# Kernel tuning notes

Measured on AMD Instinct MI355X. Metric: run time of the kernel, lower is better.

Reference implementation:

```python
import jax, jax.numpy as jnp
import numpy as np

N_NODES = 100000
N_EDGES = 1000000
F = 64
ALPHA = 0.1
BETA = 0.5


def setup_inputs() -> dict:
    key = jax.random.key(0)
    k1, k2, k3, k4, k5, k6 = jax.random.split(key, 6)
    features = jax.random.normal(k1, (N_NODES, F), dtype=jnp.float32)
    features0 = jax.random.normal(k2, (N_NODES, F), dtype=jnp.float32)
    edge_src = jax.random.randint(k3, (N_EDGES,), 0, N_NODES, dtype=jnp.int32)
    edge_dst = jax.random.randint(k4, (N_EDGES,), 0, N_NODES, dtype=jnp.int32)
    edge_vals = jax.random.uniform(k5, (N_EDGES,), dtype=jnp.float32)
    W = jax.random.normal(k6, (F, F), dtype=jnp.float32) * (1.0 / np.sqrt(F))
    return {"features": features, "features0": features0, "edge_src": edge_src,
            "edge_dst": edge_dst, "edge_vals": edge_vals, "W": W}


def reference(features, features0, edge_src, edge_dst, edge_vals, W):
    # hi = A @ features  (sparse propagation via edge-list segment sum)
    msgs = features[edge_src] * edge_vals[:, None]           # [E, F]
    hi = jax.ops.segment_sum(msgs, edge_dst, num_segments=N_NODES)  # [N, F]
    # variant=False branch of GCNII-style layer
    support = (1.0 - ALPHA) * hi + ALPHA * features0          # [N, F]
    r = support
    output = BETA * (support @ W) + (1.0 - BETA) * r          # [N, F]
    return jax.nn.relu(output)
```

## Files before the change

### kernel.cpp

```cpp
#include <hip/hip_runtime.h>

#define N_NODES 100000
#define N_EDGES 1000000
#define FDIM    64
#define TILES   6250
#define CAP     36
#define LBS     37

#define MM_BLOCKS  512
#define EPB        4096
#define BIN_BLOCKS ((N_EDGES + EPB - 1) / EPB)

#define NPART  512
#define PNODES 196
#define PCAP   2560

#define SCAN_BLOCKS 391

#define B_GCUR  0u
#define B_BKT   4096u
#define B_PRE   10489856u
#define B_GBF   23289856u
#define B_NEED  36100000u

#define C_DEG    0u
#define C_OFFS   409600u
#define C_CURSOR 819200u
#define C_BSUM   1228800u
#define C_BOFF   1232896u
#define C_BPACK  1236992u
#define C_PRE    5242880u
#define C_GBF    18042880u

typedef short bf16x8 __attribute__((ext_vector_type(8)));
typedef float f32x4  __attribute__((ext_vector_type(4)));

__device__ __forceinline__ short f2bf(float f) {
    unsigned u = __float_as_uint(f);
    u += 0x7fff + ((u >> 16) & 1);
    return (short)(u >> 16);
}

__device__ __forceinline__ unsigned packrec(int s, float v) {
    unsigned q = (unsigned)__float2int_rn(v * 32768.0f);
    q = q > 32767u ? 32767u : q;
    return ((unsigned)s << 15) | q;
}

__device__ __forceinline__ int part_of(int d) {
    return (int)(((unsigned)(d >> 2) * 171197u) >> 23);
}

__global__ __launch_bounds__(512, 4) void k_fused(
        const float* __restrict__ feat, const float* __restrict__ f0,
        const float* __restrict__ W, unsigned short* __restrict__ gbf,
        unsigned short* __restrict__ preBf,
        const int* __restrict__ src, const int* __restrict__ dst,
        const float* __restrict__ val,
        unsigned* __restrict__ bkt, int* __restrict__ gcur, int binBlocks) {

    if ((int)blockIdx.x < binBlocks) {
        __shared__ int            hist[512];
        __shared__ int            excl[512];
        __shared__ int            curs[512];
        __shared__ int            gbas[512];
        __shared__ int            wsum[8];
        __shared__ unsigned short slotpid[EPB];
        __shared__ uint2          rbuf[EPB];

        int t = threadIdx.x;
        hist[t] = 0;
        __syncthreads();

        int e0 = blockIdx.x * EPB + t * 8;
        unsigned recx[8]; int dd[8]; int pid[8];
        bool vld = e0 < N_EDGES;
        if (vld) {
            int4   sa = *(const int4*)(src + e0);
            int4   sb = *(const int4*)(src + e0 + 4);
            int4   da = *(const int4*)(dst + e0);
            int4   db = *(const int4*)(dst + e0 + 4);
            float4 va = *(const float4*)(val + e0);
            float4 vb = *(const float4*)(val + e0 + 4);
            int   s8[8] = {sa.x, sa.y, sa.z, sa.w, sb.x, sb.y, sb.z, sb.w};
            int   d8[8] = {da.x, da.y, da.z, da.w, db.x, db.y, db.z, db.w};
            float v8[8] = {va.x, va.y, va.z, va.w, vb.x, vb.y, vb.z, vb.w};
#pragma unroll
            for (int j = 0; j < 8; ++j) {
                recx[j] = packrec(s8[j], v8[j]);
                dd[j]   = d8[j];
                pid[j]  = part_of(d8[j]);
            }
#pragma unroll
            for (int j = 0; j < 8; ++j)
                atomicAdd(&hist[pid[j]], 1);
        }
        __syncthreads();

        int myv  = hist[t];
        int lanev = myv;
#pragma unroll
        for (int off = 1; off < 64; off <<= 1) {
            int nv = __shfl_up(lanev, off, 64);
            if ((t & 63) >= off) lanev += nv;
        }
        if ((t & 63) == 63) wsum[t >> 6] = lanev;
        __syncthreads();
        int prev = 0, total = 0;
#pragma unroll
        for (int w = 0; w < 8; ++w) {
            int s = wsum[w];
            prev  += (w < (t >> 6)) ? s : 0;
            total += s;
        }
        int ex = lanev + prev - myv;
        excl[t] = ex;
        curs[t] = ex;
        gbas[t] = (myv > 0) ? atomicAdd(&gcur[t], myv) : 0;
        __syncthreads();

        if (vld) {
#pragma unroll
            for (int j = 0; j < 8; ++j) {
                int pos = atomicAdd(&curs[pid[j]], 1);
                rbuf[pos]    = make_uint2(recx[j], (unsigned)dd[j]);
                slotpid[pos] = (unsigned short)pid[j];
            }
        }
        __syncthreads();

        uint2* pbuf = (uint2*)bkt;
        for (int i = t; i < total; i += 512) {
            int p   = slotpid[i];
            int off = gbas[p] + (i - excl[p]);
            if (off < PCAP)
                pbuf[(size_t)p * PCAP + off] = rbuf[i];
        }
        return;
    }

    int lane = threadIdx.x & 63;
    int mmb  = blockIdx.x - binBlocks;
    int wid  = mmb * 8 + (threadIdx.x >> 6);
    int nw   = (gridDim.x - binBlocks) * 8;
    int n16  = lane & 15, q = lane >> 4;

    bf16x8 bf[2][4];
#pragma unroll
    for (int s = 0; s < 2; ++s)
#pragma unroll
        for (int t = 0; t < 4; ++t) {
            bf16x8 b;
#pragma unroll
            for (int j = 0; j < 8; ++j) {
                int k = 32 * s + 8 * q + j, n = 16 * t + n16;
                float m = 0.5f * W[k * FDIM + n] + (k == n ? 0.5f : 0.0f);
                b[j] = f2bf(m);
            }
            bf[s][t] = b;
        }

    for (int tid = wid; tid < 2 * TILES; tid += nw) {
        bool hpath = tid >= TILES;
        int  row0  = (hpath ? tid - TILES : tid) * 16;
        const float* x = (hpath ? f0 : feat) + (size_t)row0 * FDIM;

        bf16x8 af[2];
#pragma unroll
        for (int s = 0; s < 2; ++s) {
            const float* xp = x + (size_t)n16 * FDIM + 32 * s + 8 * q;
            float4 u0 = *(const float4*)xp;
            float4 u1 = *(const float4*)(xp + 4);
            bf16x8 a;
            a[0] = f2bf(u0.x); a[1] = f2bf(u0.y); a[2] = f2bf(u0.z); a[3] = f2bf(u0.w);
            a[4] = f2bf(u1.x); a[5] = f2bf(u1.y); a[6] = f2bf(u1.z); a[7] = f2bf(u1.w);
            af[s] = a;
        }

        f32x4 acc[4] = {{0,0,0,0},{0,0,0,0},{0,0,0,0},{0,0,0,0}};
#pragma unroll
        for (int s = 0; s < 2; ++s)
#pragma unroll
            for (int t = 0; t < 4; ++t)
                acc[t] = __builtin_amdgcn_mfma_f32_16x16x32_bf16(af[s], bf[s][t], acc[t], 0, 0, 0);

        if (!hpath) {
#pragma unroll
            for (int t = 0; t < 4; ++t)
#pragma unroll
                for (int r = 0; r < 4; ++r)
                    gbf[(size_t)(row0 + 4 * q + r) * FDIM + 16 * t + n16] =
                        (unsigned short)f2bf(acc[t][r]);
        } else {
#pragma unroll
            for (int t = 0; t < 4; ++t)
#pragma unroll
                for (int r = 0; r < 4; ++r)
                    preBf[(size_t)(row0 + 4 * q + r) * FDIM + 16 * t + n16] =
                        (unsigned short)f2bf(0.1f * acc[t][r]);
        }
    }
}

__global__ __launch_bounds__(1024, 8) void k_pg(
        const unsigned* __restrict__ bkt, const int* __restrict__ gcur,
        const unsigned short* __restrict__ gbf,
        const unsigned short* __restrict__ preBf, float* __restrict__ out) {
    __shared__ int      lcnt[PNODES];
    __shared__ unsigned lbkt[PNODES * LBS];

    int p = blockIdx.x, t = threadIdx.x;
    int p196 = p * PNODES;

    for (int i = t; i < PNODES; i += 1024) lcnt[i] = 0;
    __syncthreads();

    int nE = gcur[p];
    if (nE > PCAP) nE = PCAP;
    const uint2* pb = (const uint2*)bkt + (size_t)p * PCAP;
    for (int e = t; e < nE; e += 1024) {
        uint2 r  = pb[e];
        int   ld = (int)r.y - p196;
        int  pos = atomicAdd(&lcnt[ld], 1);
        if (pos < CAP) lbkt[ld * LBS + pos] = r.x;
    }
    __syncthreads();

    int lane = t & 63, w = t >> 6;
    int fl = lane & 15, sub = lane >> 4;

    for (int ld0 = 2 * w; ld0 < PNODES; ld0 += 32) {
        int ld1   = ld0 + 1;
        int node0 = p196 + ld0;
        int node1 = p196 + ld1;
        if (node0 >= N_NODES) break;
        bool has1 = node1 < N_NODES;

        int c0 = lcnt[ld0];
        int deg0 = __builtin_amdgcn_readfirstlane(c0 < CAP ? c0 : CAP);
        int c1 = has1 ? lcnt[ld1] : 0;
        int deg1 = __builtin_amdgcn_readfirstlane(c1 < CAP ? c1 : CAP);
        int mdeg = deg0 > deg1 ? deg0 : deg1;

        uint2 hp0 = ((const uint2*)(preBf + (size_t)node0 * FDIM))[fl];
        uint2 hp1 = ((const uint2*)(preBf +
                       (size_t)(has1 ? node1 : node0) * FDIM))[fl];

        float a0 = 0, a1 = 0, a2 = 0, a3 = 0;
        float b0 = 0, b1 = 0, b2 = 0, b3 = 0;

        for (int e0 = 0; e0 < mdeg; e0 += 16) {
            unsigned rr0[4], rr1[4];
#pragma unroll
            for (int j = 0; j < 4; ++j) {
                int idx = e0 + 4 * j + sub;
                rr0[j] = (idx < deg0) ? lbkt[ld0 * LBS + idx] : 0u;
                rr1[j] = (idx < deg1) ? lbkt[ld1 * LBS + idx] : 0u;
            }
            uint2 u0[4], u1[4];
#pragma unroll
            for (int j = 0; j < 4; ++j) {
                u0[j] = ((const uint2*)(gbf + (size_t)(rr0[j] >> 15) * FDIM))[fl];
                u1[j] = ((const uint2*)(gbf + (size_t)(rr1[j] >> 15) * FDIM))[fl];
            }
#pragma unroll
            for (int j = 0; j < 4; ++j) {
                float v0 = (float)(rr0[j] & 0x7fffu) * (1.0f / 32768.0f);
                float v1 = (float)(rr1[j] & 0x7fffu) * (1.0f / 32768.0f);
                a0 = fmaf(v0, __uint_as_float(u0[j].x << 16),         a0);
                a1 = fmaf(v0, __uint_as_float(u0[j].x & 0xffff0000u), a1);
                a2 = fmaf(v0, __uint_as_float(u0[j].y << 16),         a2);
                a3 = fmaf(v0, __uint_as_float(u0[j].y & 0xffff0000u), a3);
                b0 = fmaf(v1, __uint_as_float(u1[j].x << 16),         b0);
                b1 = fmaf(v1, __uint_as_float(u1[j].x & 0xffff0000u), b1);
                b2 = fmaf(v1, __uint_as_float(u1[j].y << 16),         b2);
                b3 = fmaf(v1, __uint_as_float(u1[j].y & 0xffff0000u), b3);
            }
        }
        a0 += __shfl_xor(a0, 16); a0 += __shfl_xor(a0, 32);
        a1 += __shfl_xor(a1, 16); a1 += __shfl_xor(a1, 32);
        a2 += __shfl_xor(a2, 16); a2 += __shfl_xor(a2, 32);
        a3 += __shfl_xor(a3, 16); a3 += __shfl_xor(a3, 32);
        b0 += __shfl_xor(b0, 16); b0 += __shfl_xor(b0, 32);
        b1 += __shfl_xor(b1, 16); b1 += __shfl_xor(b1, 32);
        b2 += __shfl_xor(b2, 16); b2 += __shfl_xor(b2, 32);
        b3 += __shfl_xor(b3, 16); b3 += __shfl_xor(b3, 32);
        if (sub == 0) {
            float4 r4;
            r4.x = fmaxf(0.9f * a0 + __uint_as_float(hp0.x << 16),         0.0f);
            r4.y = fmaxf(0.9f * a1 + __uint_as_float(hp0.x & 0xffff0000u), 0.0f);
            r4.z = fmaxf(0.9f * a2 + __uint_as_float(hp0.y << 16),         0.0f);
            r4.w = fmaxf(0.9f * a3 + __uint_as_float(hp0.y & 0xffff0000u), 0.0f);
            ((float4*)(out + (size_t)node0 * FDIM))[fl] = r4;
            if (has1) {
                float4 s4;
                s4.x = fmaxf(0.9f * b0 + __uint_as_float(hp1.x << 16),         0.0f);
                s4.y = fmaxf(0.9f * b1 + __uint_as_float(hp1.x & 0xffff0000u), 0.0f);
                s4.z = fmaxf(0.9f * b2 + __uint_as_float(hp1.y << 16),         0.0f);
                s4.w = fmaxf(0.9f * b3 + __uint_as_float(hp1.y & 0xffff0000u), 0.0f);
                ((float4*)(out + (size_t)node1 * FDIM))[fl] = s4;
            }
        }
    }
}

__device__ __forceinline__ void gather_core(int node, int lane,
                                            const unsigned* base, int deg,
                                            const unsigned short* gbf,
                                            const unsigned short* preBf,
                                            float* out) {
    int fl  = lane & 31;
    int sub = lane >> 5;

    unsigned hp = ((const unsigned*)(preBf + (size_t)node * FDIM))[fl];
    float accLo = 0.0f, accHi = 0.0f;

    for (int e0 = 0; e0 < deg; e0 += 16) {
        unsigned rsel[8];
        float    vsel[8];
#pragma unroll
        for (int j = 0; j < 8; ++j) {
            int i0 = e0 + 2 * j, i1 = i0 + 1;
            int c0 = i0 < deg ? i0 : deg - 1;
            int c1 = i1 < deg ? i1 : deg - 1;
            unsigned rA = base[c0];
            unsigned rB = base[c1];
            unsigned r  = sub ? rB : rA;
            bool ok = (sub ? i1 : i0) < deg;
            rsel[j] = r;
            vsel[j] = ok ? (float)(r & 0x7fffu) * (1.0f / 32768.0f) : 0.0f;
        }
        unsigned u[8];
#pragma unroll
        for (int j = 0; j < 8; ++j)
            u[j] = *(const unsigned*)(gbf + (size_t)(rsel[j] >> 15) * FDIM + 2 * fl);
#pragma unroll
        for (int j = 0; j < 8; ++j) {
            accLo = fmaf(vsel[j], __uint_as_float(u[j] << 16), accLo);
            accHi = fmaf(vsel[j], __uint_as_float(u[j] & 0xffff0000u), accHi);
        }
    }
    accLo += __shfl_xor(accLo, 32);
    accHi += __shfl_xor(accHi, 32);
    if (sub == 0) {
        float2 r2;
        r2.x = fmaxf(0.9f * accLo + __uint_as_float(hp << 16), 0.0f);
        r2.y = fmaxf(0.9f * accHi + __uint_as_float(hp & 0xffff0000u), 0.0f);
        ((float2*)(out + (size_t)node * FDIM))[fl] = r2;
    }
}

__global__ __launch_bounds__(256, 8) void k_gather_c(
        const int* __restrict__ offs, const unsigned* __restrict__ bpack,
        const unsigned short* __restrict__ gbf,
        const unsigned short* __restrict__ preBf, float* __restrict__ out) {
    int gid  = blockIdx.x * blockDim.x + threadIdx.x;
    int node = __builtin_amdgcn_readfirstlane(gid >> 6);
    int lane = threadIdx.x & 63;
    if (node >= N_NODES) return;
    int beg = __builtin_amdgcn_readfirstlane(offs[node]);
    int end = __builtin_amdgcn_readfirstlane(
        (node == N_NODES - 1) ? N_EDGES : offs[node + 1]);
    gather_core(node, lane, bpack + beg, end - beg, gbf, preBf, out);
}

__global__ void k_hist(const int* __restrict__ dst, int* __restrict__ deg) {
    int e = blockIdx.x * blockDim.x + threadIdx.x;
    if (e < N_EDGES) atomicAdd(&deg[dst[e]], 1);
}

__global__ void k_scan1(const int* __restrict__ deg, int* __restrict__ bsum) {
    __shared__ int lds[256];
    int i = blockIdx.x * 256 + threadIdx.x;
    lds[threadIdx.x] = (i < N_NODES) ? deg[i] : 0;
    __syncthreads();
    for (int s = 128; s > 0; s >>= 1) {
        if (threadIdx.x < s) lds[threadIdx.x] += lds[threadIdx.x + s];
        __syncthreads();
    }
    if (threadIdx.x == 0) bsum[blockIdx.x] = lds[0];
}

__global__ void k_scan2(const int* __restrict__ bsum, int* __restrict__ boff) {
    __shared__ int lds[512];
    int t = threadIdx.x;
    int v = (t < SCAN_BLOCKS) ? bsum[t] : 0;
    lds[t] = v;
    __syncthreads();
    for (int off = 1; off < 512; off <<= 1) {
        int add = (t >= off) ? lds[t - off] : 0;
        __syncthreads();
        lds[t] += add;
        __syncthreads();
    }
    if (t < SCAN_BLOCKS) boff[t] = lds[t] - v;
}

__global__ void k_scan3(const int* __restrict__ deg, const int* __restrict__ boff,
                        int* __restrict__ offs, int* __restrict__ cursor) {
    __shared__ int lds[256];
    int t = threadIdx.x;
    int i = blockIdx.x * 256 + t;
    int v = (i < N_NODES) ? deg[i] : 0;
    lds[t] = v;
    __syncthreads();
    for (int off = 1; off < 256; off <<= 1) {
        int add = (t >= off) ? lds[t - off] : 0;
        __syncthreads();
        lds[t] += add;
        __syncthreads();
    }
    int excl = lds[t] - v + boff[blockIdx.x];
    if (i < N_NODES) { offs[i] = excl; cursor[i] = excl; }
}

__global__ void k_bin_c(const int* __restrict__ src, const int* __restrict__ dst,
                        const float* __restrict__ val, int* __restrict__ cursor,
                        unsigned* __restrict__ bpack) {
    int e = blockIdx.x * blockDim.x + threadIdx.x;
    if (e >= N_EDGES) return;
    int d = dst[e];
    int p = atomicAdd(&cursor[d], 1);
    bpack[p] = packrec(src[e], val[e]);
}

extern "C" void kernel_launch(void* const* d_in, const int* in_sizes, int n_in,
                              void* d_out, int out_size, void* d_ws, size_t ws_size,
                              hipStream_t stream) {
    const float* features  = (const float*)d_in[0];
    const float* features0 = (const float*)d_in[1];
    const int*   edge_src  = (const int*)d_in[2];
    const int*   edge_dst  = (const int*)d_in[3];
    const float* edge_vals = (const float*)d_in[4];
    const float* W         = (const float*)d_in[5];
    float*       out       = (float*)d_out;
    char*        ws        = (char*)d_ws;

    int eblocks = (N_EDGES + 255) / 256;
    int gblocks = (N_NODES + 3) / 4;

    if (ws_size >= B_NEED) {
        int*            gcur  = (int*)(ws + B_GCUR);
        unsigned*       bkt   = (unsigned*)(ws + B_BKT);
        unsigned short* preBf = (unsigned short*)(ws + B_PRE);
        unsigned short* gbf   = (unsigned short*)(ws + B_GBF);

        hipMemsetAsync(gcur, 0, NPART * sizeof(int), stream);
        k_fused<<<BIN_BLOCKS + MM_BLOCKS, 512, 0, stream>>>(
            features, features0, W, gbf, preBf,
            edge_src, edge_dst, edge_vals, bkt, gcur, BIN_BLOCKS);
        k_pg<<<NPART, 1024, 0, stream>>>(bkt, gcur, gbf, preBf, out);
    } else {
        int*            deg    = (int*)(ws + C_DEG);
        int*            offs   = (int*)(ws + C_OFFS);
        int*            cursor = (int*)(ws + C_CURSOR);
        int*            bsum   = (int*)(ws + C_BSUM);
        int*            boff   = (int*)(ws + C_BOFF);
        unsigned*       bpack  = (unsigned*)(ws + C_BPACK);
        unsigned short* preBf  = (unsigned short*)(ws + C_PRE);
        unsigned short* gbf    = (unsigned short*)(ws + C_GBF);

        hipMemsetAsync(deg, 0, N_NODES * sizeof(int), stream);
        k_hist<<<eblocks, 256, 0, stream>>>(edge_dst, deg);
        k_scan1<<<SCAN_BLOCKS, 256, 0, stream>>>(deg, bsum);
        k_scan2<<<1, 512, 0, stream>>>(bsum, boff);
        k_scan3<<<SCAN_BLOCKS, 256, 0, stream>>>(deg, boff, offs, cursor);
        k_bin_c<<<eblocks, 256, 0, stream>>>(edge_src, edge_dst, edge_vals, cursor, bpack);
        k_fused<<<MM_BLOCKS, 512, 0, stream>>>(
            features, features0, W, gbf, preBf,
            edge_src, edge_dst, edge_vals, (unsigned*)nullptr, (int*)nullptr, 0);
        k_gather_c<<<gblocks, 256, 0, stream>>>(offs, bpack, gbf, preBf, out);
    }
}
```

Before: 147.5 us.

## Let all blocks pull matmul tiles dynamically via a global atomic counter

Bin blocks no longer exit after scattering edges. Instead, every block of the fused kernel, bin and matmul alike, claims groups of 8 tiles from a global atomic work counter and runs the feature-transform MFMA work. The aim is to balance load so the bin blocks help finish the dense transform instead of idling, which shortens the fused kernel's tail. The cost is an atomic plus two block barriers per tile group, and the memset now also has to zero the counter.

```diff
diff --git a/kernel.cpp b/kernel.cpp
--- a/kernel.cpp
+++ b/kernel.cpp
@@ -18,6 +18,7 @@
 #define SCAN_BLOCKS 391
 
 #define B_GCUR  0u
+#define B_TCNT  2048u
 #define B_BKT   4096u
 #define B_PRE   10489856u
 #define B_GBF   23289856u
@@ -31,6 +32,7 @@
 #define C_BPACK  1236992u
 #define C_PRE    5242880u
 #define C_GBF    18042880u
+#define C_TCNT   30842880u
 
 typedef short bf16x8 __attribute__((ext_vector_type(8)));
 typedef float f32x4  __attribute__((ext_vector_type(4)));
@@ -57,7 +59,10 @@
         unsigned short* __restrict__ preBf,
         const int* __restrict__ src, const int* __restrict__ dst,
         const float* __restrict__ val,
-        unsigned* __restrict__ bkt, int* __restrict__ gcur, int binBlocks) {
+        unsigned* __restrict__ bkt, int* __restrict__ gcur,
+        int* __restrict__ tcnt, int binBlocks) {
+
+    __shared__ int tbase;
 
     if ((int)blockIdx.x < binBlocks) {
         __shared__ int            hist[512];
@@ -136,14 +141,12 @@
             if (off < PCAP)
                 pbuf[(size_t)p * PCAP + off] = rbuf[i];
         }
-        return;
+        __syncthreads();
     }
 
     int lane = threadIdx.x & 63;
-    int mmb  = blockIdx.x - binBlocks;
-    int wid  = mmb * 8 + (threadIdx.x >> 6);
-    int nw   = (gridDim.x - binBlocks) * 8;
     int n16  = lane & 15, q = lane >> 4;
+    int w    = threadIdx.x >> 6;
 
     bf16x8 bf[2][4];
 #pragma unroll
@@ -160,44 +163,53 @@
             bf[s][t] = b;
         }
 
-    for (int tid = wid; tid < 2 * TILES; tid += nw) {
-        bool hpath = tid >= TILES;
-        int  row0  = (hpath ? tid - TILES : tid) * 16;
-        const float* x = (hpath ? f0 : feat) + (size_t)row0 * FDIM;
-
-        bf16x8 af[2];
-#pragma unroll
-        for (int s = 0; s < 2; ++s) {
-            const float* xp = x + (size_t)n16 * FDIM + 32 * s + 8 * q;
-            float4 u0 = *(const float4*)xp;
-            float4 u1 = *(const float4*)(xp + 4);
-            bf16x8 a;
-            a[0] = f2bf(u0.x); a[1] = f2bf(u0.y); a[2] = f2bf(u0.z); a[3] = f2bf(u0.w);
-            a[4] = f2bf(u1.x); a[5] = f2bf(u1.y); a[6] = f2bf(u1.z); a[7] = f2bf(u1.w);
-            af[s] = a;
-        }
-
-        f32x4 acc[4] = {{0,0,0,0},{0,0,0,0},{0,0,0,0},{0,0,0,0}};
-#pragma unroll
-        for (int s = 0; s < 2; ++s)
-#pragma unroll
-            for (int t = 0; t < 4; ++t)
-                acc[t] = __builtin_amdgcn_mfma_f32_16x16x32_bf16(af[s], bf[s][t], acc[t], 0, 0, 0);
-
-        if (!hpath) {
-#pragma unroll
-            for (int t = 0; t < 4; ++t)
-#pragma unroll
-                for (int r = 0; r < 4; ++r)
-                    gbf[(size_t)(row0 + 4 * q + r) * FDIM + 16 * t + n16] =
-                        (unsigned short)f2bf(acc[t][r]);
-        } else {
-#pragma unroll
-            for (int t = 0; t < 4; ++t)
-#pragma unroll
-                for (int r = 0; r < 4; ++r)
-                    preBf[(size_t)(row0 + 4 * q + r) * FDIM + 16 * t + n16] =
-                        (unsigned short)f2bf(0.1f * acc[t][r]);
+    while (true) {
+        if (threadIdx.x == 0) tbase = atomicAdd(tcnt, 8);
+        __syncthreads();
+        int base = tbase;
+        __syncthreads();
+        if (base >= 2 * TILES) break;
+
+        int tid = base + w;
+        if (tid < 2 * TILES) {
+            bool hpath = tid >= TILES;
+            int  row0  = (hpath ? tid - TILES : tid) * 16;
+            const float* x = (hpath ? f0 : feat) + (size_t)row0 * FDIM;
+
+            bf16x8 af[2];
+#pragma unroll
+            for (int s = 0; s < 2; ++s) {
+                const float* xp = x + (size_t)n16 * FDIM + 32 * s + 8 * q;
+                float4 u0 = *(const float4*)xp;
+                float4 u1 = *(const float4*)(xp + 4);
+                bf16x8 a;
+                a[0] = f2bf(u0.x); a[1] = f2bf(u0.y); a[2] = f2bf(u0.z); a[3] = f2bf(u0.w);
+                a[4] = f2bf(u1.x); a[5] = f2bf(u1.y); a[6] = f2bf(u1.z); a[7] = f2bf(u1.w);
+                af[s] = a;
+            }
+
+            f32x4 acc[4] = {{0,0,0,0},{0,0,0,0},{0,0,0,0},{0,0,0,0}};
+#pragma unroll
+            for (int s = 0; s < 2; ++s)
+#pragma unroll
+                for (int t = 0; t < 4; ++t)
+                    acc[t] = __builtin_amdgcn_mfma_f32_16x16x32_bf16(af[s], bf[s][t], acc[t], 0, 0, 0);
+
+            if (!hpath) {
+#pragma unroll
+                for (int t = 0; t < 4; ++t)
+#pragma unroll
+                    for (int r = 0; r < 4; ++r)
+                        gbf[(size_t)(row0 + 4 * q + r) * FDIM + 16 * t + n16] =
+                            (unsigned short)f2bf(acc[t][r]);
+            } else {
+#pragma unroll
+                for (int t = 0; t < 4; ++t)
+#pragma unroll
+                    for (int r = 0; r < 4; ++r)
+                        preBf[(size_t)(row0 + 4 * q + r) * FDIM + 16 * t + n16] =
+                            (unsigned short)f2bf(0.1f * acc[t][r]);
+            }
         }
     }
 }
@@ -441,14 +453,15 @@
 
     if (ws_size >= B_NEED) {
         int*            gcur  = (int*)(ws + B_GCUR);
+        int*            tcnt  = (int*)(ws + B_TCNT);
         unsigned*       bkt   = (unsigned*)(ws + B_BKT);
         unsigned short* preBf = (unsigned short*)(ws + B_PRE);
         unsigned short* gbf   = (unsigned short*)(ws + B_GBF);
 
-        hipMemsetAsync(gcur, 0, NPART * sizeof(int), stream);
+        hipMemsetAsync(gcur, 0, 2048 + sizeof(int), stream);
         k_fused<<<BIN_BLOCKS + MM_BLOCKS, 512, 0, stream>>>(
             features, features0, W, gbf, preBf,
-            edge_src, edge_dst, edge_vals, bkt, gcur, BIN_BLOCKS);
+            edge_src, edge_dst, edge_vals, bkt, gcur, tcnt, BIN_BLOCKS);
         k_pg<<<NPART, 1024, 0, stream>>>(bkt, gcur, gbf, preBf, out);
     } else {
         int*            deg    = (int*)(ws + C_DEG);
@@ -459,8 +472,10 @@
         unsigned*       bpack  = (unsigned*)(ws + C_BPACK);
         unsigned short* preBf  = (unsigned short*)(ws + C_PRE);
         unsigned short* gbf    = (unsigned short*)(ws + C_GBF);
+        int*            tcnt   = (int*)(ws + C_TCNT);
 
         hipMemsetAsync(deg, 0, N_NODES * sizeof(int), stream);
+        hipMemsetAsync(tcnt, 0, sizeof(int), stream);
         k_hist<<<eblocks, 256, 0, stream>>>(edge_dst, deg);
         k_scan1<<<SCAN_BLOCKS, 256, 0, stream>>>(deg, bsum);
         k_scan2<<<1, 512, 0, stream>>>(bsum, boff);
@@ -468,7 +483,8 @@
         k_bin_c<<<eblocks, 256, 0, stream>>>(edge_src, edge_dst, edge_vals, cursor, bpack);
         k_fused<<<MM_BLOCKS, 512, 0, stream>>>(
             features, features0, W, gbf, preBf,
-            edge_src, edge_dst, edge_vals, (unsigned*)nullptr, (int*)nullptr, 0);
+            edge_src, edge_dst, edge_vals,
+            (unsigned*)nullptr, (int*)nullptr, tcnt, 0);
         k_gather_c<<<gblocks, 256, 0, stream>>>(offs, bpack, gbf, preBf, out);
     }
 }
```

Measured after the change: 153.6 us. 4.1% more time.
